# Kernel tuning notes

Hardware: AMD Instinct MI355X
Metric: run time of the kernel (lower is better)

Reference implementation:

```python
import jax, jax.numpy as jnp
import numpy as np

POOL = (7, 7)
A = -0.5  # Keys cubic coefficient, matches TF v2 tf.image.resize(method='bicubic')


def _cubic_weights(t):
    # t in [0,1); weights for taps at floor-1, floor, floor+1, floor+2
    t2 = t * t
    t3 = t2 * t
    wm1 = A * (t3 - 2.0 * t2 + t)
    w0 = (A + 2.0) * t3 - (A + 3.0) * t2 + 1.0
    u = 1.0 - t
    w1 = (A + 2.0) * u * u * u - (A + 3.0) * u * u + 1.0
    w2 = A * (t2 - t3)
    return jnp.stack([wm1, w0, w1, w2], axis=-1)


def _axis_taps(lo, hi, out_size, max_idx):
    # lo/hi: [B,N] integer-valued pixel crop bounds (hi exclusive).
    # Returns tap indices [B,N,out,4] int32 and cubic weights [B,N,out,4].
    span = hi - lo
    grid = (jnp.arange(out_size, dtype=jnp.float32) + 0.5) / out_size
    s = lo[..., None] + grid * span[..., None] - 0.5  # half-pixel centers
    f = jnp.floor(s)
    t = s - f
    idx = f[..., None] + jnp.arange(-1.0, 3.0)
    lo_c = lo[..., None, None]
    hi_c = jnp.maximum(hi[..., None, None] - 1.0, lo_c)
    idx = jnp.clip(jnp.clip(idx, lo_c, hi_c), 0.0, max_idx).astype(jnp.int32)
    return idx, _cubic_weights(t)


def _pool_level(fm, py1, px1, py2, px2):
    # fm: [B,H,W,C]; bounds: [B,N]. Returns [B,N,ph,pw,C].
    B, H, W, C = fm.shape
    iy, wy = _axis_taps(py1, py2, POOL[0], H - 1)  # [B,N,ph,4]
    ix, wx = _axis_taps(px1, px2, POOL[1], W - 1)  # [B,N,pw,4]
    bi = jnp.arange(B).reshape(B, 1, 1, 1, 1, 1)
    # gather the 4x4 bicubic neighborhood: [B,N,ph,pw,4,4,C]
    vals = fm[bi, iy[:, :, :, None, :, None], ix[:, :, None, :, None, :]]
    return jnp.einsum('bnik,bnjl,bnijklc->bnijc', wy, wx, vals)


def _forward(boxes, image_shape, feature_maps):
    y1, x1, y2, x2 = [boxes[..., k] for k in range(4)]
    h = y2 - y1
    w = x2 - x1
    area = (image_shape[0] * image_shape[1]).astype(jnp.float32)
    roi = jnp.log2(jnp.sqrt(h * w) / (224.0 / jnp.sqrt(area)))
    roi_level = jnp.clip(4 + jnp.round(roi).astype(jnp.int32), 2, 5)  # [B,N]
    B, N = boxes.shape[:2]
    C = feature_maps[0].shape[-1]
    out = jnp.zeros((B, N, POOL[0], POOL[1], C), dtype=feature_maps[0].dtype)
    for level, fm in zip((2, 3, 4, 5), feature_maps):
        H, W = fm.shape[1], fm.shape[2]
        scale = jnp.array([H, W, H, W], dtype=jnp.float32)
        b = jax.lax.stop_gradient(jnp.round(boxes * scale))  # denorm_box
        py1 = jnp.minimum(b[..., 0], b[..., 2])
        px1 = jnp.minimum(b[..., 1], b[..., 3])
        py2 = jnp.maximum(b[..., 0], b[..., 2])
        px2 = jnp.maximum(b[..., 1], b[..., 3])
        pooled = _pool_level(fm, py1, px1, py2, px2)
        # zero-sum denormed boxes produce zeros (per original), and only boxes
        # routed to this level contribute; final gather/sort restores original
        # box order, which masked accumulation reproduces directly.
        valid = (roi_level == level) & ((py1 + px1 + py2 + px2) != 0.0)
        out = out + pooled * valid[..., None, None, None].astype(out.dtype)
    return out


def setup_inputs() -> dict:
    key = jax.random.key(0)
    ks = jax.random.split(key, 9)
    B, N, C = 2, 200, 256
    y1 = jax.random.uniform(ks[0], (B, N)) * 0.6
    x1 = jax.random.uniform(ks[1], (B, N)) * 0.6
    hh = 0.05 + jax.random.uniform(ks[2], (B, N)) * 0.35
    ww = 0.05 + jax.random.uniform(ks[3], (B, N)) * 0.35
    boxes = jnp.stack([y1, x1, jnp.minimum(y1 + hh, 1.0), jnp.minimum(x1 + ww, 1.0)], axis=-1)
    return {
        'boxes': boxes.astype(jnp.float32),
        'image_shape': jnp.array([1024, 1024, 3], dtype=jnp.int32),
        'p2': jax.random.normal(ks[4], (B, 256, 256, C), dtype=jnp.float32),
        'p3': jax.random.normal(ks[5], (B, 128, 128, C), dtype=jnp.float32),
        'p4': jax.random.normal(ks[6], (B, 64, 64, C), dtype=jnp.float32),
        'p5': jax.random.normal(ks[7], (B, 32, 32, C), dtype=jnp.float32),
    }


def reference(boxes, image_shape, p2, p3, p4, p5):
    return _forward(boxes, image_shape, (p2, p3, p4, p5))
```

## Files before the change

kernel.cpp:

```cpp
#include <hip/hip_runtime.h>

constexpr int POOL = 7;
constexpr int NC = 256;
constexpr int CHUNK = 32;

__global__ __launch_bounds__(256)
void roi_align_row_kernel(const float* __restrict__ boxes,
                          const int*   __restrict__ ishape,
                          const float* __restrict__ p2,
                          const float* __restrict__ p3,
                          const float* __restrict__ p4,
                          const float* __restrict__ p5,
                          float*       __restrict__ out,
                          int B, int N)
{
    __shared__ float vy[CHUNK][NC];

    int blk = blockIdx.x;
    int i = blk % POOL;
    int n = (blk / POOL) % N;
    int b = blk / (POOL * N);
    int c = threadIdx.x;

    const float* bp = boxes + 4 * (b * N + n);
    float y1 = bp[0], x1 = bp[1], y2 = bp[2], x2 = bp[3];

    float area  = (float)(ishape[0] * ishape[1]);
    float denom = 224.0f / sqrtf(area);
    float roi   = log2f(sqrtf((y2 - y1) * (x2 - x1)) / denom);
    int lvl = 4 + (int)rintf(roi);
    lvl = lvl < 2 ? 2 : (lvl > 5 ? 5 : lvl);

    const float* fm; int H;
    if      (lvl == 2) { fm = p2; H = 256; }
    else if (lvl == 3) { fm = p3; H = 128; }
    else if (lvl == 4) { fm = p4; H = 64;  }
    else               { fm = p5; H = 32;  }
    const int W = H;
    const float Hf = (float)H, Wf = (float)W;

    float by1 = rintf(y1 * Hf), bx1 = rintf(x1 * Wf);
    float by2 = rintf(y2 * Hf), bx2 = rintf(x2 * Wf);
    float py1 = fminf(by1, by2), px1 = fminf(bx1, bx2);
    float py2 = fmaxf(by1, by2), px2 = fmaxf(bx1, bx2);

    size_t obase = (size_t)blk * POOL * NC + (size_t)c;

    if (py1 + px1 + py2 + px2 == 0.0f) {
        #pragma unroll
        for (int j = 0; j < POOL; ++j) out[obase + (size_t)j * NC] = 0.0f;
        return;
    }

    const float A = -0.5f;

    int iy[4]; float wy[4];
    {
        float span = py2 - py1;
        float grid = ((float)i + 0.5f) / (float)POOL;
        float s = py1 + grid * span - 0.5f;
        float f = floorf(s);
        float t = s - f;
        float hi_c = fmaxf(py2 - 1.0f, py1);
        float maxi = Hf - 1.0f;
        #pragma unroll
        for (int k = 0; k < 4; ++k) {
            float idx = f + (float)(k - 1);
            idx = fminf(fmaxf(idx, py1), hi_c);
            idx = fminf(fmaxf(idx, 0.0f), maxi);
            iy[k] = (int)idx;
        }
        float t2 = t * t, t3 = t2 * t;
        float u = 1.0f - t, u2 = u * u, u3 = u2 * u;
        wy[0] = A * (t3 - 2.0f * t2 + t);
        wy[1] = (A + 2.0f) * t3 - (A + 3.0f) * t2 + 1.0f;
        wy[2] = (A + 2.0f) * u3 - (A + 3.0f) * u2 + 1.0f;
        wy[3] = A * (t2 - t3);
    }

    int   ix[POOL][4];
    float wx[POOL][4];
    {
        float span = px2 - px1;
        float hi_c = fmaxf(px2 - 1.0f, px1);
        float maxi = Wf - 1.0f;
        #pragma unroll
        for (int j = 0; j < POOL; ++j) {
            float grid = ((float)j + 0.5f) / (float)POOL;
            float s = px1 + grid * span - 0.5f;
            float f = floorf(s);
            float t = s - f;
            #pragma unroll
            for (int l = 0; l < 4; ++l) {
                float idx = f + (float)(l - 1);
                idx = fminf(fmaxf(idx, px1), hi_c);
                idx = fminf(fmaxf(idx, 0.0f), maxi);
                ix[j][l] = (int)idx;
            }
            float t2 = t * t, t3 = t2 * t;
            float u = 1.0f - t, u2 = u * u, u3 = u2 * u;
            wx[j][0] = A * (t3 - 2.0f * t2 + t);
            wx[j][1] = (A + 2.0f) * t3 - (A + 3.0f) * t2 + 1.0f;
            wx[j][2] = (A + 2.0f) * u3 - (A + 3.0f) * u2 + 1.0f;
            wx[j][3] = A * (t2 - t3);
        }
    }

    int x_lo = ix[0][0];
    int x_hi = ix[POOL - 1][3];

    const float* row0 = fm + ((size_t)b * H + iy[0]) * (size_t)(W * NC) + c;
    const float* row1 = fm + ((size_t)b * H + iy[1]) * (size_t)(W * NC) + c;
    const float* row2 = fm + ((size_t)b * H + iy[2]) * (size_t)(W * NC) + c;
    const float* row3 = fm + ((size_t)b * H + iy[3]) * (size_t)(W * NC) + c;

    float acc[POOL];
    #pragma unroll
    for (int j = 0; j < POOL; ++j) acc[j] = 0.0f;

    for (int x0 = x_lo; x0 <= x_hi; x0 += CHUNK) {
        int xe = x0 + CHUNK - 1;
        if (xe > x_hi) xe = x_hi;

        if (x0 > x_lo) __syncthreads();

        for (int x = x0; x <= xe; ++x) {
            size_t o = (size_t)x * NC;
            float v = wy[0] * row0[o] + wy[1] * row1[o]
                    + wy[2] * row2[o] + wy[3] * row3[o];
            vy[x - x0][c] = v;
        }
        __syncthreads();

        #pragma unroll
        for (int j = 0; j < POOL; ++j) {
            #pragma unroll
            for (int l = 0; l < 4; ++l) {
                int xr = ix[j][l] - x0;
                if (xr >= 0 && xr <= xe - x0)
                    acc[j] += wx[j][l] * vy[xr][c];
            }
        }
    }

    #pragma unroll
    for (int j = 0; j < POOL; ++j)
        out[obase + (size_t)j * NC] = acc[j];
}

extern "C" void kernel_launch(void* const* d_in, const int* in_sizes, int n_in,
                              void* d_out, int out_size, void* d_ws, size_t ws_size,
                              hipStream_t stream) {
    const float* boxes  = (const float*)d_in[0];
    const int*   ishape = (const int*)d_in[1];
    const float* p2     = (const float*)d_in[2];
    const float* p3     = (const float*)d_in[3];
    const float* p4     = (const float*)d_in[4];
    const float* p5     = (const float*)d_in[5];
    float* out = (float*)d_out;

    int B = in_sizes[2] / (256 * 256 * 256);
    int N = in_sizes[0] / (4 * B);

    int blocks = B * N * POOL;
    roi_align_row_kernel<<<blocks, 256, 0, stream>>>(boxes, ishape, p2, p3, p4, p5, out, B, N);
}
```

Measured before the change: 241.0 us.

## Map one wavefront per output row with float4 channels and register-only accumulation

Each 64-lane wavefront now handles one pooled output row, and every lane covers four channels through float4 loads and stores. Four rows share a 256-thread block. The shared-memory staging and block barriers are gone; each vertically interpolated column is computed in registers and its horizontal weight is applied right away, with the next column prefetched in software. This aims to cut synchronisation and load-instruction overhead and to raise memory-level parallelism, at the cost of a per-column scan over all 28 tap indices.

```diff
diff --git a/kernel.cpp b/kernel.cpp
--- a/kernel.cpp
+++ b/kernel.cpp
@@ -2,25 +2,25 @@
 
 constexpr int POOL = 7;
 constexpr int NC = 256;
-constexpr int CHUNK = 32;
 
 __global__ __launch_bounds__(256)
-void roi_align_row_kernel(const float* __restrict__ boxes,
-                          const int*   __restrict__ ishape,
-                          const float* __restrict__ p2,
-                          const float* __restrict__ p3,
-                          const float* __restrict__ p4,
-                          const float* __restrict__ p5,
-                          float*       __restrict__ out,
-                          int B, int N)
+void roi_align_wave_row(const float* __restrict__ boxes,
+                        const int*   __restrict__ ishape,
+                        const float* __restrict__ p2,
+                        const float* __restrict__ p3,
+                        const float* __restrict__ p4,
+                        const float* __restrict__ p5,
+                        float*       __restrict__ out,
+                        int N, int nrows)
 {
-    __shared__ float vy[CHUNK][NC];
+    int row  = (blockIdx.x << 2) + (threadIdx.x >> 6);
+    if (row >= nrows) return;
+    int lane = threadIdx.x & 63;
 
-    int blk = blockIdx.x;
-    int i = blk % POOL;
-    int n = (blk / POOL) % N;
-    int b = blk / (POOL * N);
-    int c = threadIdx.x;
+    int i  = row % POOL;
+    int bn = row / POOL;
+    int n  = bn % N;
+    int b  = bn / N;
 
     const float* bp = boxes + 4 * (b * N + n);
     float y1 = bp[0], x1 = bp[1], y2 = bp[2], x2 = bp[3];
@@ -44,11 +44,13 @@
     float py1 = fminf(by1, by2), px1 = fminf(bx1, bx2);
     float py2 = fmaxf(by1, by2), px2 = fmaxf(bx1, bx2);
 
-    size_t obase = (size_t)blk * POOL * NC + (size_t)c;
+    float* obase = out + (size_t)row * (POOL * NC) + (size_t)lane * 4;
 
     if (py1 + px1 + py2 + px2 == 0.0f) {
+        float4 z = {0.f, 0.f, 0.f, 0.f};
         #pragma unroll
-        for (int j = 0; j < POOL; ++j) out[obase + (size_t)j * NC] = 0.0f;
+        for (int j = 0; j < POOL; ++j)
+            *(float4*)(obase + (size_t)j * NC) = z;
         return;
     }
 
@@ -109,43 +111,55 @@
     int x_lo = ix[0][0];
     int x_hi = ix[POOL - 1][3];
 
-    const float* row0 = fm + ((size_t)b * H + iy[0]) * (size_t)(W * NC) + c;
-    const float* row1 = fm + ((size_t)b * H + iy[1]) * (size_t)(W * NC) + c;
-    const float* row2 = fm + ((size_t)b * H + iy[2]) * (size_t)(W * NC) + c;
-    const float* row3 = fm + ((size_t)b * H + iy[3]) * (size_t)(W * NC) + c;
+    const size_t rstride = (size_t)(W * NC);
+    const float* r0 = fm + ((size_t)b * H + iy[0]) * rstride + (size_t)lane * 4;
+    const float* r1 = fm + ((size_t)b * H + iy[1]) * rstride + (size_t)lane * 4;
+    const float* r2 = fm + ((size_t)b * H + iy[2]) * rstride + (size_t)lane * 4;
+    const float* r3 = fm + ((size_t)b * H + iy[3]) * rstride + (size_t)lane * 4;
 
-    float acc[POOL];
+    float4 acc[POOL];
     #pragma unroll
-    for (int j = 0; j < POOL; ++j) acc[j] = 0.0f;
+    for (int j = 0; j < POOL; ++j) acc[j] = make_float4(0.f, 0.f, 0.f, 0.f);
 
-    for (int x0 = x_lo; x0 <= x_hi; x0 += CHUNK) {
-        int xe = x0 + CHUNK - 1;
-        if (xe > x_hi) xe = x_hi;
+    size_t o = (size_t)x_lo * NC;
+    float4 n0 = *(const float4*)(r0 + o);
+    float4 n1 = *(const float4*)(r1 + o);
+    float4 n2 = *(const float4*)(r2 + o);
+    float4 n3 = *(const float4*)(r3 + o);
 
-        if (x0 > x_lo) __syncthreads();
-
-        for (int x = x0; x <= xe; ++x) {
-            size_t o = (size_t)x * NC;
-            float v = wy[0] * row0[o] + wy[1] * row1[o]
-                    + wy[2] * row2[o] + wy[3] * row3[o];
-            vy[x - x0][c] = v;
+    for (int x = x_lo; x <= x_hi; ++x) {
+        float4 c0 = n0, c1 = n1, c2 = n2, c3 = n3;
+        if (x < x_hi) {
+            size_t on = (size_t)(x + 1) * NC;
+            n0 = *(const float4*)(r0 + on);
+            n1 = *(const float4*)(r1 + on);
+            n2 = *(const float4*)(r2 + on);
+            n3 = *(const float4*)(r3 + on);
         }
-        __syncthreads();
+        float4 v;
+        v.x = wy[0] * c0.x + wy[1] * c1.x + wy[2] * c2.x + wy[3] * c3.x;
+        v.y = wy[0] * c0.y + wy[1] * c1.y + wy[2] * c2.y + wy[3] * c3.y;
+        v.z = wy[0] * c0.z + wy[1] * c1.z + wy[2] * c2.z + wy[3] * c3.z;
+        v.w = wy[0] * c0.w + wy[1] * c1.w + wy[2] * c2.w + wy[3] * c3.w;
 
         #pragma unroll
         for (int j = 0; j < POOL; ++j) {
+            float w = 0.f;
             #pragma unroll
-            for (int l = 0; l < 4; ++l) {
-                int xr = ix[j][l] - x0;
-                if (xr >= 0 && xr <= xe - x0)
-                    acc[j] += wx[j][l] * vy[xr][c];
+            for (int l = 0; l < 4; ++l)
+                if (x == ix[j][l]) w += wx[j][l];
+            if (w != 0.f) {
+                acc[j].x += w * v.x;
+                acc[j].y += w * v.y;
+                acc[j].z += w * v.z;
+                acc[j].w += w * v.w;
             }
         }
     }
 
     #pragma unroll
     for (int j = 0; j < POOL; ++j)
-        out[obase + (size_t)j * NC] = acc[j];
+        *(float4*)(obase + (size_t)j * NC) = acc[j];
 }
 
 extern "C" void kernel_launch(void* const* d_in, const int* in_sizes, int n_in,
@@ -162,6 +176,8 @@
     int B = in_sizes[2] / (256 * 256 * 256);
     int N = in_sizes[0] / (4 * B);
 
-    int blocks = B * N * POOL;
-    roi_align_row_kernel<<<blocks, 256, 0, stream>>>(boxes, ishape, p2, p3, p4, p5, out, B, N);
+    int nrows  = B * N * POOL;
+    int blocks = (nrows + 3) / 4;
+    roi_align_wave_row<<<blocks, 256, 0, stream>>>(boxes, ishape, p2, p3, p4, p5,
+                                                   out, N, nrows);
 }
```

New measurement: 233.3 us. -3.2%, faster.
